# Optimization experiments

Measured on AMD Instinct MI355X. Metric: run time of the kernel, lower is better.

Reference implementation:

```python
import jax, jax.numpy as jnp
import numpy as np

N_SRC = 100000
N_DST = 20000
N_EDGES = 640000
D_IN = 128
D_OUT = 128


def setup_inputs() -> dict:
    key = jax.random.key(0)
    ks = jax.random.split(key, 6)
    feat_src = jax.random.normal(ks[0], (N_SRC, D_IN), dtype=jnp.float32)
    feat_dst = jax.random.normal(ks[1], (N_DST, D_IN), dtype=jnp.float32)
    src_idx = jax.random.randint(ks[2], (N_EDGES,), 0, N_SRC, dtype=jnp.int64 if jax.config.jax_enable_x64 else jnp.int32)
    dst_idx = jax.random.randint(ks[3], (N_EDGES,), 0, N_DST, dtype=jnp.int64 if jax.config.jax_enable_x64 else jnp.int32)
    # xavier-uniform-ish init scale for [out, in] Linear weights
    lim = float(np.sqrt(6.0 / (D_IN + D_OUT)))
    W_self = jax.random.uniform(ks[4], (D_OUT, D_IN), jnp.float32, -lim, lim)
    W_neigh = jax.random.uniform(ks[5], (D_OUT, D_IN), jnp.float32, -lim, lim)
    b_self = jnp.zeros((D_OUT,), jnp.float32)
    b_neigh = jnp.zeros((D_OUT,), jnp.float32)
    return {
        "feat_src": feat_src, "feat_dst": feat_dst,
        "src_idx": src_idx, "dst_idx": dst_idx,
        "W_self": W_self, "b_self": b_self,
        "W_neigh": W_neigh, "b_neigh": b_neigh,
    }


def reference(feat_src, feat_dst, src_idx, dst_idx, W_self, b_self, W_neigh, b_neigh):
    n_dst = feat_dst.shape[0]
    # message passing: copy_src + mean reduce over incoming edges per dst node
    msgs = feat_src[src_idx]                                   # [E, D_in]
    summed = jax.ops.segment_sum(msgs, dst_idx, num_segments=n_dst)  # [N_dst, D_in]
    deg = jax.ops.segment_sum(jnp.ones((src_idx.shape[0],), feat_src.dtype),
                              dst_idx, num_segments=n_dst)     # [N_dst]
    h_neigh = summed / jnp.maximum(deg, 1.0)[:, None]          # mean (0 for isolated)
    # rst = fc_self(h_self) + fc_neigh(h_neigh); no activation
    rst = (feat_dst @ W_self.T + b_self) + (h_neigh @ W_neigh.T + b_neigh)
    return rst
```

## Files before the change

### kernel.cpp

```cpp
#include <hip/hip_runtime.h>

#define D 128
#define NDST 20000
#define NHB 64
#define CAP 96

typedef __attribute__((ext_vector_type(8))) short short8;
typedef __attribute__((ext_vector_type(4))) float f32x4;
typedef __attribute__((ext_vector_type(2))) float f32x2;

__device__ __forceinline__ unsigned f2bf(float f) {
  unsigned x = __float_as_uint(f);
  return (x + 0x7FFFu + ((x >> 16) & 1u)) >> 16;
}
__device__ __forceinline__ unsigned pack2(float a, float b) {
  return f2bf(a) | (f2bf(b) << 16);
}
__device__ __forceinline__ unsigned pack_fp8x4(float a, float b, float c, float d) {
  int v = 0;
  v = __builtin_amdgcn_cvt_pk_fp8_f32(a, b, v, false);
  v = __builtin_amdgcn_cvt_pk_fp8_f32(c, d, v, true);
  return (unsigned)v;
}

__global__ __launch_bounds__(512) void k1(
    const int* __restrict__ dst_idx,
    const float* __restrict__ feat_src,
    const float* __restrict__ feat_dst,
    const float* __restrict__ W_self,
    const float* __restrict__ b_self,
    const float* __restrict__ b_neigh,
    unsigned char* __restrict__ hist8,
    unsigned char* __restrict__ rank8,
    unsigned char* __restrict__ fsrc8,
    float* __restrict__ out,
    int n_src, int n_dst, int n_edges, int EPB, int NCB)
{
  __shared__ __align__(16) unsigned char ldsb[43520];
  const int tid = threadIdx.x;
  const int bid = blockIdx.x;

  if (bid < NHB) {
    unsigned int* hist = reinterpret_cast<unsigned int*>(ldsb);
    for (int i = tid; i < NDST / 16; i += 512)
      reinterpret_cast<uint4*>(hist)[i] = make_uint4(0u, 0u, 0u, 0u);
    __syncthreads();
    const int e0 = bid * EPB;
    const int e1 = min(e0 + EPB, n_edges);
    for (int e = e0 + tid; e < e1; e += 512) {
      int d = dst_idx[e];
      int sh = (d & 3) << 3;
      unsigned old = atomicAdd(&hist[d >> 2], 1u << sh);
      rank8[e] = (unsigned char)((old >> sh) & 0xFFu);
    }
    __syncthreads();
    uint4* rowp = reinterpret_cast<uint4*>(hist8 + (size_t)bid * NDST);
    const uint4* h4 = reinterpret_cast<const uint4*>(hist);
    for (int i = tid; i < NDST / 16; i += 512) rowp[i] = h4[i];
  } else if (bid < NHB + NCB) {
    const long long NCONV = (long long)n_src * 16;
    const long long NU = NCONV + 16;
    const long long stride = (long long)NCB * 512;
    long long u = (long long)(bid - NHB) * 512 + tid;
    for (; u < NU; u += stride) {
      if (u < NCONV) {
        long long e = u * 8;
        const float4* p = reinterpret_cast<const float4*>(feat_src + e);
        float4 a = p[0], b = p[1];
        uint2 o;
        o.x = pack_fp8x4(a.x, a.y, a.z, a.w);
        o.y = pack_fp8x4(b.x, b.y, b.z, b.w);
        *reinterpret_cast<uint2*>(fsrc8 + e) = o;
      } else {
        *reinterpret_cast<uint2*>(fsrc8 + (size_t)n_src * D + (u - NCONV) * 8) =
            make_uint2(0u, 0u);
      }
    }
  } else {
    unsigned short (*As)[136] = reinterpret_cast<unsigned short (*)[136]>(ldsb);
    unsigned short (*Bs)[136] =
        reinterpret_cast<unsigned short (*)[136]>(ldsb + 32 * 136 * 2);
    const int w = tid >> 6;
    const int lane = tid & 63;
    const int row0 = (bid - NHB - NCB) * 32;

    {
      int r = tid >> 4;
      int q = tid & 15;
      int gr = row0 + r;
      uint4 o = make_uint4(0u, 0u, 0u, 0u);
      if (gr < n_dst) {
        const float4* p = reinterpret_cast<const float4*>(
            feat_dst + (size_t)gr * D + q * 8);
        float4 a = p[0], b = p[1];
        o.x = pack2(a.x, a.y); o.y = pack2(a.z, a.w);
        o.z = pack2(b.x, b.y); o.w = pack2(b.z, b.w);
      }
      *reinterpret_cast<uint4*>(&As[r][q * 8]) = o;
    }
    {
      int n = tid >> 2;
      int q = tid & 3;
      const float4* p = reinterpret_cast<const float4*>(
          W_self + (size_t)n * D + q * 32);
      #pragma unroll
      for (int h = 0; h < 4; ++h) {
        float4 a = p[2 * h], b = p[2 * h + 1];
        uint4 o;
        o.x = pack2(a.x, a.y); o.y = pack2(a.z, a.w);
        o.z = pack2(b.x, b.y); o.w = pack2(b.z, b.w);
        *reinterpret_cast<uint4*>(&Bs[n][q * 32 + h * 8]) = o;
      }
    }
    __syncthreads();

    const int m  = w & 1;
    const int n0 = (w >> 1) * 2;
    const int ar = m * 16 + (lane & 15);
    const int kb = (lane >> 4) * 8;
    f32x4 acc2[2];
    acc2[0] = (f32x4){0.f, 0.f, 0.f, 0.f};
    acc2[1] = (f32x4){0.f, 0.f, 0.f, 0.f};
    #pragma unroll
    for (int kh = 0; kh < 4; ++kh) {
      short8 a = *reinterpret_cast<const short8*>(&As[ar][kh * 32 + kb]);
      #pragma unroll
      for (int t2 = 0; t2 < 2; ++t2) {
        short8 b = *reinterpret_cast<const short8*>(
            &Bs[(n0 + t2) * 16 + (lane & 15)][kh * 32 + kb]);
        acc2[t2] = __builtin_amdgcn_mfma_f32_16x16x32_bf16(a, b, acc2[t2], 0, 0, 0);
      }
    }
    const int r0 = row0 + m * 16 + (lane >> 4) * 4;
    #pragma unroll
    for (int t2 = 0; t2 < 2; ++t2) {
      int col = (n0 + t2) * 16 + (lane & 15);
      float bv = b_self[col] + b_neigh[col];
      #pragma unroll
      for (int r = 0; r < 4; ++r) {
        int gr = r0 + r;
        if (gr < n_dst) out[(size_t)gr * D + col] = acc2[t2][r] + bv;
      }
    }
  }
}

__global__ __launch_bounds__(256) void pB(
    unsigned char* __restrict__ hist8,
    int* __restrict__ degi,
    int n_dst)
{
  int d = blockIdx.x * 256 + threadIdx.x;
  if (d >= n_dst) return;
  unsigned char* col = hist8 + d;
  unsigned run = 0;
  #pragma unroll 8
  for (int b = 0; b < NHB; ++b) {
    unsigned h = col[(size_t)b * NDST];
    col[(size_t)b * NDST] = (unsigned char)run;
    run += h;
  }
  degi[d] = (int)run;
}

__global__ __launch_bounds__(256) void p3(
    const int* __restrict__ src_idx,
    const int* __restrict__ dst_idx,
    const unsigned char* __restrict__ rank8,
    const unsigned char* __restrict__ blockBase8,
    int* __restrict__ bucket,
    int n_edges, int EPB)
{
  int e0 = (blockIdx.x * 256 + threadIdx.x) * 4;
  if (e0 >= n_edges) return;
  if (e0 + 4 <= n_edges) {
    int4 s4 = *reinterpret_cast<const int4*>(src_idx + e0);
    int4 d4 = *reinterpret_cast<const int4*>(dst_idx + e0);
    uchar4 r4 = *reinterpret_cast<const uchar4*>(rank8 + e0);
    int ds[4] = {d4.x, d4.y, d4.z, d4.w};
    int ss[4] = {s4.x, s4.y, s4.z, s4.w};
    unsigned rr[4] = {r4.x, r4.y, r4.z, r4.w};
    #pragma unroll
    for (int j = 0; j < 4; ++j) {
      int hb = (e0 + j) / EPB;
      unsigned slot = (unsigned)blockBase8[(size_t)hb * NDST + ds[j]] + rr[j];
      if (slot < CAP) bucket[(size_t)ds[j] * CAP + slot] = ss[j];
    }
  } else {
    for (int e = e0; e < n_edges; ++e) {
      int d = dst_idx[e];
      int hb = e / EPB;
      unsigned slot = (unsigned)blockBase8[(size_t)hb * NDST + d] + rank8[e];
      if (slot < CAP) bucket[(size_t)d * CAP + slot] = src_idx[e];
    }
  }
}

__global__ __launch_bounds__(512) void tail(
    const unsigned char* __restrict__ fsrc8,
    const int* __restrict__ degi,
    const int* __restrict__ bucket,
    const float* __restrict__ W_neigh,
    float* __restrict__ out,
    int n_src, int n_dst)
{
  __shared__ unsigned short Ah[32][136];
  __shared__ unsigned short Bs[128][136];

  const int tid  = threadIdx.x;
  const int w    = tid >> 6;
  const int lane = tid & 63;
  const int row0 = blockIdx.x * 32;

  {
    int n = tid >> 2;
    int q = tid & 3;
    const float4* p = reinterpret_cast<const float4*>(
        W_neigh + (size_t)n * D + q * 32);
    #pragma unroll
    for (int h = 0; h < 4; ++h) {
      float4 a = p[2 * h], b = p[2 * h + 1];
      uint4 o;
      o.x = pack2(a.x, a.y); o.y = pack2(a.z, a.w);
      o.z = pack2(b.x, b.y); o.w = pack2(b.z, b.w);
      *reinterpret_cast<uint4*>(&Bs[n][q * 32 + h * 8]) = o;
    }
  }

  {
    const int g = lane >> 4;
    const int c = lane & 15;
    const uint2* fs2 = reinterpret_cast<const uint2*>(fsrc8);

    for (int it = 0; it < 4; ++it) {
      int row = w * 4 + it;
      int gr = row0 + row;
      if (gr >= n_dst) {
        if (lane < 16)
          *reinterpret_cast<uint4*>(&Ah[row][c * 8]) = make_uint4(0u,0u,0u,0u);
        continue;
      }
      const int total = degi[gr];
      const int use = min(total, CAP);
      const int* brow = bucket + (size_t)gr * CAP;

      float acc[8];
      #pragma unroll
      for (int j = 0; j < 8; ++j) acc[j] = 0.f;

      for (int i = g; i < use; i += 32) {
        int s[8];
        #pragma unroll
        for (int k = 0; k < 8; ++k)
          s[k] = (i + 4 * k < use) ? brow[i + 4 * k] : n_src;
        uint2 v[8];
        #pragma unroll
        for (int k = 0; k < 8; ++k)
          v[k] = fs2[(size_t)s[k] * 16 + c];
        #pragma unroll
        for (int k = 0; k < 8; ++k) {
          f32x2 a0 = __builtin_amdgcn_cvt_pk_f32_fp8(v[k].x, false);
          f32x2 a1 = __builtin_amdgcn_cvt_pk_f32_fp8(v[k].x, true);
          f32x2 a2 = __builtin_amdgcn_cvt_pk_f32_fp8(v[k].y, false);
          f32x2 a3 = __builtin_amdgcn_cvt_pk_f32_fp8(v[k].y, true);
          acc[0] += a0.x; acc[1] += a0.y; acc[2] += a1.x; acc[3] += a1.y;
          acc[4] += a2.x; acc[5] += a2.y; acc[6] += a3.x; acc[7] += a3.y;
        }
      }

      #pragma unroll
      for (int j = 0; j < 8; ++j) {
        acc[j] += __shfl_xor(acc[j], 16);
        acc[j] += __shfl_xor(acc[j], 32);
      }

      if (lane < 16) {
        float inv = 1.0f / fmaxf((float)total, 1.0f);
        uint4 o;
        o.x = pack2(acc[0] * inv, acc[1] * inv);
        o.y = pack2(acc[2] * inv, acc[3] * inv);
        o.z = pack2(acc[4] * inv, acc[5] * inv);
        o.w = pack2(acc[6] * inv, acc[7] * inv);
        *reinterpret_cast<uint4*>(&Ah[row][c * 8]) = o;
      }
    }
  }
  __syncthreads();

  const int m  = w & 1;
  const int n0 = (w >> 1) * 2;
  const int ar = m * 16 + (lane & 15);
  const int kb = (lane >> 4) * 8;

  f32x4 acc2[2];
  acc2[0] = (f32x4){0.f, 0.f, 0.f, 0.f};
  acc2[1] = (f32x4){0.f, 0.f, 0.f, 0.f};

  #pragma unroll
  for (int kh = 0; kh < 4; ++kh) {
    short8 a = *reinterpret_cast<const short8*>(&Ah[ar][kh * 32 + kb]);
    #pragma unroll
    for (int t2 = 0; t2 < 2; ++t2) {
      short8 b = *reinterpret_cast<const short8*>(
          &Bs[(n0 + t2) * 16 + (lane & 15)][kh * 32 + kb]);
      acc2[t2] = __builtin_amdgcn_mfma_f32_16x16x32_bf16(a, b, acc2[t2], 0, 0, 0);
    }
  }

  const int r0 = row0 + m * 16 + (lane >> 4) * 4;
  #pragma unroll
  for (int t2 = 0; t2 < 2; ++t2) {
    int col = (n0 + t2) * 16 + (lane & 15);
    #pragma unroll
    for (int r = 0; r < 4; ++r) {
      int gr = r0 + r;
      if (gr < n_dst) {
        size_t idx = (size_t)gr * D + col;
        out[idx] = out[idx] + acc2[t2][r];
      }
    }
  }
}

extern "C" void kernel_launch(void* const* d_in, const int* in_sizes, int n_in,
                              void* d_out, int out_size, void* d_ws, size_t ws_size,
                              hipStream_t stream) {
  const float* feat_src = (const float*)d_in[0];
  const float* feat_dst = (const float*)d_in[1];
  const int*   src_idx  = (const int*)d_in[2];
  const int*   dst_idx  = (const int*)d_in[3];
  const float* W_self   = (const float*)d_in[4];
  const float* b_self   = (const float*)d_in[5];
  const float* W_neigh  = (const float*)d_in[6];
  const float* b_neigh  = (const float*)d_in[7];
  float* out = (float*)d_out;

  const int n_src   = in_sizes[0] / D;
  const int n_dst   = in_sizes[1] / D;
  const int n_edges = in_sizes[2];

  unsigned char* fsrc8 = (unsigned char*)d_ws;
  int* degi   = (int*)(fsrc8 + (size_t)(n_src + 1) * D);
  int* bucket = degi + NDST;
  unsigned char* rank8 = (unsigned char*)(bucket + (size_t)NDST * CAP);
  unsigned char* hist8 = rank8 + (((size_t)n_edges + 15) & ~(size_t)15);

  const int EPB = (n_edges + NHB - 1) / NHB;
  const int NCB = 256;
  const int NG  = (n_dst + 31) / 32;

  k1<<<NHB + NCB + NG, 512, 0, stream>>>(
      dst_idx, feat_src, feat_dst, W_self, b_self, b_neigh,
      hist8, rank8, fsrc8, out, n_src, n_dst, n_edges, EPB, NCB);

  pB<<<(n_dst + 255) / 256, 256, 0, stream>>>(hist8, degi, n_dst);

  p3<<<(n_edges / 4 + 255) / 256, 256, 0, stream>>>(
      src_idx, dst_idx, rank8, hist8, bucket, n_edges, EPB);

  tail<<<NG, 512, 0, stream>>>(
      fsrc8, degi, bucket, W_neigh, out, n_src, n_dst);
}
```

Measured before the change: 65.32 us.

## Transpose per-block histogram and fold prefix scan into consumers, dropping scan kernel

The per-block destination histogram is now stored transposed (dst-major, 64 bytes per destination), so the separate prefix-scan kernel pB is removed. The scatter kernel computes each edge's base offset by reading the 64-byte row and summing the bytes of earlier blocks with SAD byte sums, and the tail kernel recomputes the degree the same way. This saves one kernel launch and a strided column pass, at the cost of 64-byte reads per edge in p3, redundant per-edge summation, and uncoalesced byte-scattered writes of the histogram in k1.

```diff
diff --git a/kernel.cpp b/kernel.cpp
--- a/kernel.cpp
+++ b/kernel.cpp
@@ -21,6 +21,13 @@
   v = __builtin_amdgcn_cvt_pk_fp8_f32(a, b, v, false);
   v = __builtin_amdgcn_cvt_pk_fp8_f32(c, d, v, true);
   return (unsigned)v;
+}
+__device__ __forceinline__ unsigned bytesum(unsigned w, unsigned acc) {
+#if __has_builtin(__builtin_amdgcn_sad_u8)
+  return __builtin_amdgcn_sad_u8(w, 0u, acc);
+#else
+  return acc + (w & 0xFFu) + ((w >> 8) & 0xFFu) + ((w >> 16) & 0xFFu) + (w >> 24);
+#endif
 }
 
 __global__ __launch_bounds__(512) void k1(
@@ -30,7 +37,7 @@
     const float* __restrict__ W_self,
     const float* __restrict__ b_self,
     const float* __restrict__ b_neigh,
-    unsigned char* __restrict__ hist8,
+    unsigned char* __restrict__ hist8T,
     unsigned char* __restrict__ rank8,
     unsigned char* __restrict__ fsrc8,
     float* __restrict__ out,
@@ -54,9 +61,10 @@
       rank8[e] = (unsigned char)((old >> sh) & 0xFFu);
     }
     __syncthreads();
-    uint4* rowp = reinterpret_cast<uint4*>(hist8 + (size_t)bid * NDST);
-    const uint4* h4 = reinterpret_cast<const uint4*>(hist);
-    for (int i = tid; i < NDST / 16; i += 512) rowp[i] = h4[i];
+    for (int d = tid; d < NDST; d += 512) {
+      unsigned byte = (hist[d >> 2] >> ((d & 3) << 3)) & 0xFFu;
+      hist8T[(size_t)d * NHB + bid] = (unsigned char)byte;
+    }
   } else if (bid < NHB + NCB) {
     const long long NCONV = (long long)n_src * 16;
     const long long NU = NCONV + 16;
@@ -145,34 +153,19 @@
   }
 }
 
-__global__ __launch_bounds__(256) void pB(
-    unsigned char* __restrict__ hist8,
-    int* __restrict__ degi,
-    int n_dst)
-{
-  int d = blockIdx.x * 256 + threadIdx.x;
-  if (d >= n_dst) return;
-  unsigned char* col = hist8 + d;
-  unsigned run = 0;
-  #pragma unroll 8
-  for (int b = 0; b < NHB; ++b) {
-    unsigned h = col[(size_t)b * NDST];
-    col[(size_t)b * NDST] = (unsigned char)run;
-    run += h;
-  }
-  degi[d] = (int)run;
-}
-
 __global__ __launch_bounds__(256) void p3(
     const int* __restrict__ src_idx,
     const int* __restrict__ dst_idx,
     const unsigned char* __restrict__ rank8,
-    const unsigned char* __restrict__ blockBase8,
+    const unsigned char* __restrict__ hist8T,
     int* __restrict__ bucket,
     int n_edges, int EPB)
 {
   int e0 = (blockIdx.x * 256 + threadIdx.x) * 4;
   if (e0 >= n_edges) return;
+  const int hb0 = e0 / EPB;
+  const int rem = e0 - hb0 * EPB;
+
   if (e0 + 4 <= n_edges) {
     int4 s4 = *reinterpret_cast<const int4*>(src_idx + e0);
     int4 d4 = *reinterpret_cast<const int4*>(dst_idx + e0);
@@ -182,15 +175,32 @@
     unsigned rr[4] = {r4.x, r4.y, r4.z, r4.w};
     #pragma unroll
     for (int j = 0; j < 4; ++j) {
-      int hb = (e0 + j) / EPB;
-      unsigned slot = (unsigned)blockBase8[(size_t)hb * NDST + ds[j]] + rr[j];
+      int hb = hb0 + (((rem + j) >= EPB) ? 1 : 0);
+      const uint4* rp = reinterpret_cast<const uint4*>(
+          hist8T + (size_t)ds[j] * NHB);
+      uint4 h0 = rp[0], h1 = rp[1], h2 = rp[2], h3 = rp[3];
+      unsigned wd[16] = {h0.x, h0.y, h0.z, h0.w, h1.x, h1.y, h1.z, h1.w,
+                         h2.x, h2.y, h2.z, h2.w, h3.x, h3.y, h3.z, h3.w};
+      unsigned base = 0;
+      #pragma unroll
+      for (int t = 0; t < 16; ++t) {
+        int c = hb - t * 4;
+        if (c > 0) {
+          unsigned word = wd[t];
+          if (c < 4) word &= (0xFFFFFFFFu >> ((4 - c) << 3));
+          base = bytesum(word, base);
+        }
+      }
+      unsigned slot = base + rr[j];
       if (slot < CAP) bucket[(size_t)ds[j] * CAP + slot] = ss[j];
     }
   } else {
     for (int e = e0; e < n_edges; ++e) {
       int d = dst_idx[e];
       int hb = e / EPB;
-      unsigned slot = (unsigned)blockBase8[(size_t)hb * NDST + d] + rank8[e];
+      unsigned base = 0;
+      for (int b = 0; b < hb; ++b) base += hist8T[(size_t)d * NHB + b];
+      unsigned slot = base + rank8[e];
       if (slot < CAP) bucket[(size_t)d * CAP + slot] = src_idx[e];
     }
   }
@@ -198,7 +208,7 @@
 
 __global__ __launch_bounds__(512) void tail(
     const unsigned char* __restrict__ fsrc8,
-    const int* __restrict__ degi,
+    const unsigned char* __restrict__ hist8T,
     const int* __restrict__ bucket,
     const float* __restrict__ W_neigh,
     float* __restrict__ out,
@@ -240,7 +250,18 @@
           *reinterpret_cast<uint4*>(&Ah[row][c * 8]) = make_uint4(0u,0u,0u,0u);
         continue;
       }
-      const int total = degi[gr];
+      const uint4* rp = reinterpret_cast<const uint4*>(hist8T + (size_t)gr * NHB);
+      uint4 h0 = rp[0], h1 = rp[1], h2 = rp[2], h3 = rp[3];
+      unsigned dv = 0;
+      dv = bytesum(h0.x, dv); dv = bytesum(h0.y, dv);
+      dv = bytesum(h0.z, dv); dv = bytesum(h0.w, dv);
+      dv = bytesum(h1.x, dv); dv = bytesum(h1.y, dv);
+      dv = bytesum(h1.z, dv); dv = bytesum(h1.w, dv);
+      dv = bytesum(h2.x, dv); dv = bytesum(h2.y, dv);
+      dv = bytesum(h2.z, dv); dv = bytesum(h2.w, dv);
+      dv = bytesum(h3.x, dv); dv = bytesum(h3.y, dv);
+      dv = bytesum(h3.z, dv); dv = bytesum(h3.w, dv);
+      const int total = (int)dv;
       const int use = min(total, CAP);
       const int* brow = bucket + (size_t)gr * CAP;
 
@@ -340,10 +361,9 @@
   const int n_edges = in_sizes[2];
 
   unsigned char* fsrc8 = (unsigned char*)d_ws;
-  int* degi   = (int*)(fsrc8 + (size_t)(n_src + 1) * D);
-  int* bucket = degi + NDST;
+  int* bucket = (int*)(fsrc8 + (size_t)(n_src + 1) * D);
   unsigned char* rank8 = (unsigned char*)(bucket + (size_t)NDST * CAP);
-  unsigned char* hist8 = rank8 + (((size_t)n_edges + 15) & ~(size_t)15);
+  unsigned char* hist8T = rank8 + (((size_t)n_edges + 63) & ~(size_t)63);
 
   const int EPB = (n_edges + NHB - 1) / NHB;
   const int NCB = 256;
@@ -351,13 +371,11 @@
 
   k1<<<NHB + NCB + NG, 512, 0, stream>>>(
       dst_idx, feat_src, feat_dst, W_self, b_self, b_neigh,
-      hist8, rank8, fsrc8, out, n_src, n_dst, n_edges, EPB, NCB);
-
-  pB<<<(n_dst + 255) / 256, 256, 0, stream>>>(hist8, degi, n_dst);
+      hist8T, rank8, fsrc8, out, n_src, n_dst, n_edges, EPB, NCB);
 
   p3<<<(n_edges / 4 + 255) / 256, 256, 0, stream>>>(
-      src_idx, dst_idx, rank8, hist8, bucket, n_edges, EPB);
+      src_idx, dst_idx, rank8, hist8T, bucket, n_edges, EPB);
 
   tail<<<NG, 512, 0, stream>>>(
-      fsrc8, degi, bucket, W_neigh, out, n_src, n_dst);
-}
+      fsrc8, hist8T, bucket, W_neigh, out, n_src, n_dst);
+}
```

After: 79.89 us. 1.22x slower.

## Drop per-edge rank array; recompute slots with LDS atomics in scatter pass

Applied to the files above, without the earlier changes.

The histogram pass no longer records a per-edge rank byte. The scatter pass now runs one 1024-thread block per histogram block. Each block loads its exclusive-prefix row into LDS and takes bucket slots with packed byte atomics. This removes the rank8 write and read and a global gather of blockBase8 per edge, but the scatter now uses only 64 blocks with LDS atomic contention instead of a wide grid. Slot order within a dst differs from before, but the mean is unchanged.

```diff
diff --git a/kernel.cpp b/kernel.cpp
--- a/kernel.cpp
+++ b/kernel.cpp
@@ -31,7 +31,6 @@
     const float* __restrict__ b_self,
     const float* __restrict__ b_neigh,
     unsigned char* __restrict__ hist8,
-    unsigned char* __restrict__ rank8,
     unsigned char* __restrict__ fsrc8,
     float* __restrict__ out,
     int n_src, int n_dst, int n_edges, int EPB, int NCB)
@@ -49,9 +48,7 @@
     const int e1 = min(e0 + EPB, n_edges);
     for (int e = e0 + tid; e < e1; e += 512) {
       int d = dst_idx[e];
-      int sh = (d & 3) << 3;
-      unsigned old = atomicAdd(&hist[d >> 2], 1u << sh);
-      rank8[e] = (unsigned char)((old >> sh) & 0xFFu);
+      atomicAdd(&hist[d >> 2], 1u << ((d & 3) << 3));
     }
     __syncthreads();
     uint4* rowp = reinterpret_cast<uint4*>(hist8 + (size_t)bid * NDST);
@@ -163,36 +160,29 @@
   degi[d] = (int)run;
 }
 
-__global__ __launch_bounds__(256) void p3(
+__global__ __launch_bounds__(1024) void p3(
     const int* __restrict__ src_idx,
     const int* __restrict__ dst_idx,
-    const unsigned char* __restrict__ rank8,
     const unsigned char* __restrict__ blockBase8,
     int* __restrict__ bucket,
     int n_edges, int EPB)
 {
-  int e0 = (blockIdx.x * 256 + threadIdx.x) * 4;
-  if (e0 >= n_edges) return;
-  if (e0 + 4 <= n_edges) {
-    int4 s4 = *reinterpret_cast<const int4*>(src_idx + e0);
-    int4 d4 = *reinterpret_cast<const int4*>(dst_idx + e0);
-    uchar4 r4 = *reinterpret_cast<const uchar4*>(rank8 + e0);
-    int ds[4] = {d4.x, d4.y, d4.z, d4.w};
-    int ss[4] = {s4.x, s4.y, s4.z, s4.w};
-    unsigned rr[4] = {r4.x, r4.y, r4.z, r4.w};
-    #pragma unroll
-    for (int j = 0; j < 4; ++j) {
-      int hb = (e0 + j) / EPB;
-      unsigned slot = (unsigned)blockBase8[(size_t)hb * NDST + ds[j]] + rr[j];
-      if (slot < CAP) bucket[(size_t)ds[j] * CAP + slot] = ss[j];
-    }
-  } else {
-    for (int e = e0; e < n_edges; ++e) {
-      int d = dst_idx[e];
-      int hb = e / EPB;
-      unsigned slot = (unsigned)blockBase8[(size_t)hb * NDST + d] + rank8[e];
-      if (slot < CAP) bucket[(size_t)d * CAP + slot] = src_idx[e];
-    }
+  __shared__ unsigned int cur[NDST / 4];
+  const int tid = threadIdx.x;
+  const int bid = blockIdx.x;
+  const uint4* rowp = reinterpret_cast<const uint4*>(
+      blockBase8 + (size_t)bid * NDST);
+  uint4* c4 = reinterpret_cast<uint4*>(cur);
+  for (int i = tid; i < NDST / 16; i += 1024) c4[i] = rowp[i];
+  __syncthreads();
+  const int e0 = bid * EPB;
+  const int e1 = min(e0 + EPB, n_edges);
+  for (int e = e0 + tid; e < e1; e += 1024) {
+    int d = dst_idx[e];
+    int s = src_idx[e];
+    int sh = (d & 3) << 3;
+    unsigned slot = (atomicAdd(&cur[d >> 2], 1u << sh) >> sh) & 0xFFu;
+    if (slot < CAP) bucket[(size_t)d * CAP + slot] = s;
   }
 }
 
@@ -342,8 +332,7 @@
   unsigned char* fsrc8 = (unsigned char*)d_ws;
   int* degi   = (int*)(fsrc8 + (size_t)(n_src + 1) * D);
   int* bucket = degi + NDST;
-  unsigned char* rank8 = (unsigned char*)(bucket + (size_t)NDST * CAP);
-  unsigned char* hist8 = rank8 + (((size_t)n_edges + 15) & ~(size_t)15);
+  unsigned char* hist8 = (unsigned char*)(bucket + (size_t)NDST * CAP);
 
   const int EPB = (n_edges + NHB - 1) / NHB;
   const int NCB = 256;
@@ -351,12 +340,12 @@
 
   k1<<<NHB + NCB + NG, 512, 0, stream>>>(
       dst_idx, feat_src, feat_dst, W_self, b_self, b_neigh,
-      hist8, rank8, fsrc8, out, n_src, n_dst, n_edges, EPB, NCB);
+      hist8, fsrc8, out, n_src, n_dst, n_edges, EPB, NCB);
 
   pB<<<(n_dst + 255) / 256, 256, 0, stream>>>(hist8, degi, n_dst);
 
-  p3<<<(n_edges / 4 + 255) / 256, 256, 0, stream>>>(
-      src_idx, dst_idx, rank8, hist8, bucket, n_edges, EPB);
+  p3<<<NHB, 1024, 0, stream>>>(
+      src_idx, dst_idx, hist8, bucket, n_edges, EPB);
 
   tail<<<NG, 512, 0, stream>>>(
       fsrc8, degi, bucket, W_neigh, out, n_src, n_dst);
```

New measurement: 68.25 us (median of 3 runs). +4.5%, slower.
